# Kernel optimization log

Hardware: AMD Instinct MI355X
Metric: run time of the kernel (lower is better)

The kernel has to match this reference:

```python
import jax, jax.numpy as jnp
import numpy as np

EPS = 1e-8
LN_EPS = 1e-5

def _layernorm(x, g, b):
    mu = jnp.mean(x, axis=-1, keepdims=True)
    var = jnp.mean((x - mu) ** 2, axis=-1, keepdims=True)
    return (x - mu) / jnp.sqrt(var + LN_EPS) * g + b

def setup_inputs() -> dict:
    key = jax.random.key(0)
    ks = jax.random.split(key, 10)
    B, S = 8192, 4096
    input_dim, hidden_dim = 4, 256
    h4 = hidden_dim // 4  # 64
    price_series = jax.random.uniform(ks[0], (B, S, 1), dtype=jnp.float32) + 0.5
    # 4 parallel encoders stacked on leading axis: Linear(input_dim->h4) + LayerNorm(h4)
    enc_w = jax.random.normal(ks[1], (4, input_dim, h4), dtype=jnp.float32) * 0.5
    enc_b = jax.random.normal(ks[2], (4, h4), dtype=jnp.float32) * 0.02
    enc_g = jnp.ones((4, h4), dtype=jnp.float32)
    enc_beta = jnp.zeros((4, h4), dtype=jnp.float32)
    # regime head: Linear(hidden_dim->64) + ReLU + (Dropout eval=identity) + Linear(64->4)
    head_w1 = jax.random.normal(ks[3], (hidden_dim, 64), dtype=jnp.float32) * 0.0625
    head_b1 = jnp.zeros((64,), dtype=jnp.float32)
    head_w2 = jax.random.normal(ks[4], (64, 4), dtype=jnp.float32) * 0.125
    head_b2 = jnp.zeros((4,), dtype=jnp.float32)
    return {"price_series": price_series, "enc_w": enc_w, "enc_b": enc_b,
            "enc_g": enc_g, "enc_beta": enc_beta,
            "head_w1": head_w1, "head_b1": head_b1,
            "head_w2": head_w2, "head_b2": head_b2}

def reference(price_series, enc_w, enc_b, enc_g, enc_beta, head_w1, head_b1, head_w2, head_b2):
    prices = price_series[:, :, 0]  # [B, S]
    B, S = prices.shape
    # Rolling SMA(20) with clamped window start, via cumsum (single pass, no per-step loop)
    csum = jnp.concatenate([jnp.zeros((B, 1), prices.dtype), jnp.cumsum(prices, axis=1)], axis=1)  # [B, S+1]
    i = jnp.arange(S)
    start20 = jnp.maximum(0, i - 19)
    cnt20 = (i - start20 + 1).astype(prices.dtype)
    sma20 = (csum[:, i + 1] - csum[:, start20]) / cnt20  # [B, S]
    trend_signal = (prices - sma20) / (sma20 + EPS)
    f_trend = jnp.mean(trend_signal, axis=1, keepdims=True)  # [B,1]
    # momentum over last 10 steps
    p_last = prices[:, -1:]
    p_m10 = prices[:, -10:-9]
    f_mom = (p_last - p_m10) / (p_m10 + EPS)  # [B,1]
    # mean reversion
    p_mean = jnp.mean(prices, axis=1, keepdims=True)
    f_mr = (p_last - p_mean) / (p_mean + EPS)  # [B,1]
    # cycle: coefficient of variation (torch.std is unbiased, ddof=1)
    f_cyc = jnp.std(prices, axis=1, ddof=1, keepdims=True) / (p_mean + EPS)  # [B,1]
    combined = jnp.concatenate([f_trend, f_mom, f_mr, f_cyc], axis=1)  # [B, 4]
    # 4 parallel encoders: Linear -> ReLU -> LayerNorm
    pre = jnp.einsum('bi,eio->ebo', combined, enc_w) + enc_b[:, None, :]  # [4, B, 64]
    feats = _layernorm(jax.nn.relu(pre), enc_g[:, None, :], enc_beta[:, None, :])  # [4, B, 64]
    # concat order: trend, momentum, mean_rev, cycle along feature dim
    regime_features = jnp.transpose(feats, (1, 0, 2)).reshape(B, -1)  # [B, 256]
    h = jax.nn.relu(regime_features @ head_w1 + head_b1)
    regime_probs = jax.nn.softmax(h @ head_w2 + head_b2, axis=1)  # [B, 4]
    return (regime_features, regime_probs)
```

## Files before the change

kernel.cpp:

```cpp
#include <hip/hip_runtime.h>

#define EPS 1e-8f
#define LN_EPS 1e-5f
#define NROWS 8192
#define SLEN 4096
#define PROBS_OFF 2097152

typedef __attribute__((ext_vector_type(8))) short bf16x8;
typedef __attribute__((ext_vector_type(4))) float f32x4;

__device__ __forceinline__ short f2bf(float f) {
    unsigned u = __float_as_uint(f);
    unsigned r = (u + 0x7FFFu + ((u >> 16) & 1u)) >> 16;
    return (short)r;
}

#define SLP(i) ((i) + ((((i) >> 4)) << 2))

__global__ __launch_bounds__(256) void k_feat(const float* __restrict__ prices,
                                              float* __restrict__ ws) {
    __shared__ float sld[2596];
    __shared__ float red[12];

    const int t = threadIdx.x;
    const int b = blockIdx.x >> 1, h = blockIdx.x & 1;
    const int lane = t & 63, wv = t >> 6;
    const float4* rowp4 = (const float4*)(prices + (size_t)b * SLEN);

    {
        int f0 = t, f1 = t + 256;
        int g0 = 512 * h - 8 + f0, g1 = 512 * h - 8 + f1;
        float4 v0 = (g0 >= 0) ? rowp4[g0] : make_float4(0.f, 0.f, 0.f, 0.f);
        float4 v1 = rowp4[g1];
        *(float4*)&sld[SLP(4 * f0)] = v0;
        *(float4*)&sld[SLP(4 * f1)] = v1;
        if (t < 8) {
            int f2 = 512 + t;
            *(float4*)&sld[SLP(4 * f2)] = rowp4[512 * h - 8 + f2];
        }
    }
    __syncthreads();

    const int li0 = 32 + 8 * t;
    float4 s0 = *(const float4*)&sld[SLP(li0)];
    float4 s1 = *(const float4*)&sld[SLP(li0 + 4)];
    float4 q0 = *(const float4*)&sld[SLP(li0 - 20)];
    float4 q1 = *(const float4*)&sld[SLP(li0 - 16)];
    float4 q2 = *(const float4*)&sld[SLP(li0 - 12)];
    float4 q3 = *(const float4*)&sld[SLP(li0 - 8)];
    float4 q4 = *(const float4*)&sld[SLP(li0 - 4)];

    float xv[8] = { s0.x, s0.y, s0.z, s0.w, s1.x, s1.y, s1.z, s1.w };
    float ov[8] = { q0.x, q0.y, q0.z, q0.w, q1.x, q1.y, q1.z, q1.w };

    float W = q0.y + q0.z + q0.w
            + q1.x + q1.y + q1.z + q1.w
            + q2.x + q2.y + q2.z + q2.w
            + q3.x + q3.y + q3.z + q3.w
            + q4.x + q4.y + q4.z + q4.w;

    const float pf = (float)(2048 * h + 8 * t);
    float sum = 0.0f, sq = 0.0f, ts = 0.0f;
    #pragma unroll
    for (int j = 0; j < 8; ++j) {
        float x = xv[j];
        W += (j == 0) ? x : (x - ov[j]);
        sum += x;
        sq = fmaf(x, x, sq);
        float c = fminf(pf + (float)(j + 1), 20.0f);
        float num = fmaf(x, c, -W);
        float den = fmaf(EPS, c, W);
        ts += num * __builtin_amdgcn_rcpf(den);
    }

    if (h == 1 && t == 254) ws[(size_t)b * 8 + 6] = xv[6];
    if (h == 1 && t == 255) ws[(size_t)b * 8 + 7] = xv[7];

    #pragma unroll
    for (int off = 32; off > 0; off >>= 1) {
        sum += __shfl_xor(sum, off);
        sq  += __shfl_xor(sq,  off);
        ts  += __shfl_xor(ts,  off);
    }
    if (lane == 0) { red[wv * 3] = sum; red[wv * 3 + 1] = sq; red[wv * 3 + 2] = ts; }
    __syncthreads();

    if (t == 0) {
        float S = red[0] + red[3] + red[6] + red[9];
        float Q = red[1] + red[4] + red[7] + red[10];
        float T = red[2] + red[5] + red[8] + red[11];
        float* wp = ws + (size_t)b * 8 + 3 * h;
        wp[0] = S; wp[1] = Q; wp[2] = T;
    }
}

#define ROWS 32

__global__ __launch_bounds__(256) void k_head(
    const float* __restrict__ ws, float* __restrict__ out,
    const float* __restrict__ enc_w, const float* __restrict__ enc_b,
    const float* __restrict__ enc_g, const float* __restrict__ enc_bt,
    const float* __restrict__ w1, const float* __restrict__ b1,
    const float* __restrict__ w2, const float* __restrict__ b2)
{
    __shared__ float comb[ROWS][4];
    __shared__ short rfb[ROWS][264];
    __shared__ float hbuf[ROWS][68];

    const int t = threadIdx.x;
    const int r0 = blockIdx.x * ROWS;
    const int lane = t & 63, wave = t >> 6;
    const int l15 = lane & 15, q = lane >> 4;

    if (t < ROWS) {
        const float* wp = ws + (size_t)(r0 + t) * 8;
        float4 a = *(const float4*)wp;
        float4 bb = *(const float4*)(wp + 4);
        float S = a.x + a.w, Q = a.y + bb.x, T = a.z + bb.y;
        float p_m10 = bb.z, p_last = bb.w;
        float mean = S * (1.0f / 4096.0f);
        float var  = fmaxf((Q - 4096.0f * mean * mean) * (1.0f / 4095.0f), 0.0f);
        comb[t][0] = T * (1.0f / 4096.0f);
        comb[t][1] = (p_last - p_m10) / (p_m10 + EPS);
        comb[t][2] = (p_last - mean) / (mean + EPS);
        comb[t][3] = sqrtf(var) / (mean + EPS);
    }

    bf16x8 bfrag[8];
    #pragma unroll
    for (int kt = 0; kt < 8; ++kt) {
        #pragma unroll
        for (int j = 0; j < 8; ++j) {
            int k = kt * 32 + q * 8 + j;
            bfrag[kt][j] = f2bf(w1[k * 64 + wave * 16 + l15]);
        }
    }

    const float ew0 = enc_w[wave * 256 + lane];
    const float ew1v = enc_w[wave * 256 + 64 + lane];
    const float ew2v = enc_w[wave * 256 + 128 + lane];
    const float ew3v = enc_w[wave * 256 + 192 + lane];
    const float ebv = enc_b[t], egv = enc_g[t], btv = enc_bt[t];

    __syncthreads();

    for (int r = 0; r < ROWS; r += 2) {
        float4 cba = *(const float4*)comb[r];
        float4 cbb = *(const float4*)comb[r + 1];
        float va = fmaf(cba.x, ew0, fmaf(cba.y, ew1v, fmaf(cba.z, ew2v, fmaf(cba.w, ew3v, ebv))));
        float vb = fmaf(cbb.x, ew0, fmaf(cbb.y, ew1v, fmaf(cbb.z, ew2v, fmaf(cbb.w, ew3v, ebv))));
        va = fmaxf(va, 0.0f);
        vb = fmaxf(vb, 0.0f);
        float sma = va, smb = vb;
        #pragma unroll
        for (int off = 32; off > 0; off >>= 1) {
            sma += __shfl_xor(sma, off);
            smb += __shfl_xor(smb, off);
        }
        float mua = sma * (1.0f / 64.0f);
        float mub = smb * (1.0f / 64.0f);
        float da = va - mua, db = vb - mub;
        float vsa = da * da, vsb = db * db;
        #pragma unroll
        for (int off = 32; off > 0; off >>= 1) {
            vsa += __shfl_xor(vsa, off);
            vsb += __shfl_xor(vsb, off);
        }
        float ya = fmaf(da * rsqrtf(vsa * (1.0f / 64.0f) + LN_EPS), egv, btv);
        float yb = fmaf(db * rsqrtf(vsb * (1.0f / 64.0f) + LN_EPS), egv, btv);
        out[(size_t)(r0 + r) * 256 + t] = ya;
        out[(size_t)(r0 + r + 1) * 256 + t] = yb;
        rfb[r][t] = f2bf(ya);
        rfb[r + 1][t] = f2bf(yb);
    }
    __syncthreads();

    f32x4 acc0 = {0.f, 0.f, 0.f, 0.f}, acc1 = {0.f, 0.f, 0.f, 0.f};
    #pragma unroll
    for (int kt = 0; kt < 8; ++kt) {
        bf16x8 a0 = *(const bf16x8*)&rfb[l15][kt * 32 + q * 8];
        bf16x8 a1 = *(const bf16x8*)&rfb[16 + l15][kt * 32 + q * 8];
        acc0 = __builtin_amdgcn_mfma_f32_16x16x32_bf16(a0, bfrag[kt], acc0, 0, 0, 0);
        acc1 = __builtin_amdgcn_mfma_f32_16x16x32_bf16(a1, bfrag[kt], acc1, 0, 0, 0);
    }

    const int col = wave * 16 + l15;
    const float b1v = b1[col];
    #pragma unroll
    for (int rg = 0; rg < 4; ++rg) {
        hbuf[q * 4 + rg][col]      = fmaxf(acc0[rg] + b1v, 0.0f);
        hbuf[16 + q * 4 + rg][col] = fmaxf(acc1[rg] + b1v, 0.0f);
    }
    __syncthreads();

    if (t < 128) {
        int r = t >> 2, c = t & 3;
        float lg = b2[c];
        #pragma unroll
        for (int j = 0; j < 64; ++j) lg = fmaf(hbuf[r][j], w2[j * 4 + c], lg);
        float mx = fmaxf(lg, __shfl_xor(lg, 1, 4));
        mx = fmaxf(mx, __shfl_xor(mx, 2, 4));
        float ex = __expf(lg - mx);
        float s2 = ex + __shfl_xor(ex, 1, 4);
        s2 += __shfl_xor(s2, 2, 4);
        out[PROBS_OFF + (size_t)(r0 + r) * 4 + c] = ex / s2;
    }
}

extern "C" void kernel_launch(void* const* d_in, const int* in_sizes, int n_in,
                              void* d_out, int out_size, void* d_ws, size_t ws_size,
                              hipStream_t stream) {
    const float* prices  = (const float*)d_in[0];
    const float* enc_w   = (const float*)d_in[1];
    const float* enc_b   = (const float*)d_in[2];
    const float* enc_g   = (const float*)d_in[3];
    const float* enc_bt  = (const float*)d_in[4];
    const float* head_w1 = (const float*)d_in[5];
    const float* head_b1 = (const float*)d_in[6];
    const float* head_w2 = (const float*)d_in[7];
    const float* head_b2 = (const float*)d_in[8];
    float* out = (float*)d_out;
    float* ws  = (float*)d_ws;

    k_feat<<<NROWS * 2, 256, 0, stream>>>(prices, ws);
    k_head<<<NROWS / ROWS, 256, 0, stream>>>(ws, out, enc_w, enc_b, enc_g, enc_bt,
                                             head_w1, head_b1, head_w2, head_b2);
}
```

Before: 215.7 us.

## Process one row per feature block with direct global loads and fused finalize

The feature kernel now handles a full row per 512-thread block. Each thread reads its current and lookback float4s straight from global memory, relying on cache for the overlapping window loads instead of staging through LDS. The per-row feature finalization moves into this kernel, so the head kernel reads one float4 per row. The head kernel also shrinks to 16 rows per block with a single MFMA accumulator, doubling block count, and splits the w2 dot product into four independent chains. Redundant overlapping global loads may add cache traffic.

Result: slower. 307.1 us (+42.3%).

```diff
diff --git a/kernel.cpp b/kernel.cpp
--- a/kernel.cpp
+++ b/kernel.cpp
@@ -15,40 +15,24 @@
     return (short)r;
 }
 
-#define SLP(i) ((i) + ((((i) >> 4)) << 2))
-
-__global__ __launch_bounds__(256) void k_feat(const float* __restrict__ prices,
+__global__ __launch_bounds__(512) void k_feat(const float* __restrict__ prices,
                                               float* __restrict__ ws) {
-    __shared__ float sld[2596];
-    __shared__ float red[12];
+    __shared__ float red[8][3];
+    __shared__ float tailv[2];
 
     const int t = threadIdx.x;
-    const int b = blockIdx.x >> 1, h = blockIdx.x & 1;
+    const int b = blockIdx.x;
     const int lane = t & 63, wv = t >> 6;
-    const float4* rowp4 = (const float4*)(prices + (size_t)b * SLEN);
-
-    {
-        int f0 = t, f1 = t + 256;
-        int g0 = 512 * h - 8 + f0, g1 = 512 * h - 8 + f1;
-        float4 v0 = (g0 >= 0) ? rowp4[g0] : make_float4(0.f, 0.f, 0.f, 0.f);
-        float4 v1 = rowp4[g1];
-        *(float4*)&sld[SLP(4 * f0)] = v0;
-        *(float4*)&sld[SLP(4 * f1)] = v1;
-        if (t < 8) {
-            int f2 = 512 + t;
-            *(float4*)&sld[SLP(4 * f2)] = rowp4[512 * h - 8 + f2];
-        }
-    }
-    __syncthreads();
-
-    const int li0 = 32 + 8 * t;
-    float4 s0 = *(const float4*)&sld[SLP(li0)];
-    float4 s1 = *(const float4*)&sld[SLP(li0 + 4)];
-    float4 q0 = *(const float4*)&sld[SLP(li0 - 20)];
-    float4 q1 = *(const float4*)&sld[SLP(li0 - 16)];
-    float4 q2 = *(const float4*)&sld[SLP(li0 - 12)];
-    float4 q3 = *(const float4*)&sld[SLP(li0 - 8)];
-    float4 q4 = *(const float4*)&sld[SLP(li0 - 4)];
+    const float4* R4 = (const float4*)(prices + (size_t)b * SLEN);
+
+    const float4 z4 = make_float4(0.f, 0.f, 0.f, 0.f);
+    float4 s0 = R4[2 * t];
+    float4 s1 = R4[2 * t + 1];
+    float4 q0 = (2 * t - 5 >= 0) ? R4[2 * t - 5] : z4;
+    float4 q1 = (2 * t - 4 >= 0) ? R4[2 * t - 4] : z4;
+    float4 q2 = (2 * t - 3 >= 0) ? R4[2 * t - 3] : z4;
+    float4 q3 = (2 * t - 2 >= 0) ? R4[2 * t - 2] : z4;
+    float4 q4 = (2 * t - 1 >= 0) ? R4[2 * t - 1] : z4;
 
     float xv[8] = { s0.x, s0.y, s0.z, s0.w, s1.x, s1.y, s1.z, s1.w };
     float ov[8] = { q0.x, q0.y, q0.z, q0.w, q1.x, q1.y, q1.z, q1.w };
@@ -59,7 +43,7 @@
             + q3.x + q3.y + q3.z + q3.w
             + q4.x + q4.y + q4.z + q4.w;
 
-    const float pf = (float)(2048 * h + 8 * t);
+    const float pf = (float)(8 * t);
     float sum = 0.0f, sq = 0.0f, ts = 0.0f;
     #pragma unroll
     for (int j = 0; j < 8; ++j) {
@@ -73,8 +57,8 @@
         ts += num * __builtin_amdgcn_rcpf(den);
     }
 
-    if (h == 1 && t == 254) ws[(size_t)b * 8 + 6] = xv[6];
-    if (h == 1 && t == 255) ws[(size_t)b * 8 + 7] = xv[7];
+    if (t == 510) tailv[0] = xv[6];
+    if (t == 511) tailv[1] = xv[7];
 
     #pragma unroll
     for (int off = 32; off > 0; off >>= 1) {
@@ -82,19 +66,26 @@
         sq  += __shfl_xor(sq,  off);
         ts  += __shfl_xor(ts,  off);
     }
-    if (lane == 0) { red[wv * 3] = sum; red[wv * 3 + 1] = sq; red[wv * 3 + 2] = ts; }
+    if (lane == 0) { red[wv][0] = sum; red[wv][1] = sq; red[wv][2] = ts; }
     __syncthreads();
 
     if (t == 0) {
-        float S = red[0] + red[3] + red[6] + red[9];
-        float Q = red[1] + red[4] + red[7] + red[10];
-        float T = red[2] + red[5] + red[8] + red[11];
-        float* wp = ws + (size_t)b * 8 + 3 * h;
-        wp[0] = S; wp[1] = Q; wp[2] = T;
-    }
-}
-
-#define ROWS 32
+        float S = 0.f, Q = 0.f, T = 0.f;
+        #pragma unroll
+        for (int w = 0; w < 8; ++w) { S += red[w][0]; Q += red[w][1]; T += red[w][2]; }
+        float mean = S * (1.0f / 4096.0f);
+        float var  = fmaxf((Q - 4096.0f * mean * mean) * (1.0f / 4095.0f), 0.0f);
+        float p_m10 = tailv[0], p_last = tailv[1];
+        float4 f;
+        f.x = T * (1.0f / 4096.0f);
+        f.y = (p_last - p_m10) / (p_m10 + EPS);
+        f.z = (p_last - mean) / (mean + EPS);
+        f.w = sqrtf(var) / (mean + EPS);
+        ((float4*)ws)[b] = f;
+    }
+}
+
+#define ROWS 16
 
 __global__ __launch_bounds__(256) void k_head(
     const float* __restrict__ ws, float* __restrict__ out,
@@ -112,19 +103,7 @@
     const int lane = t & 63, wave = t >> 6;
     const int l15 = lane & 15, q = lane >> 4;
 
-    if (t < ROWS) {
-        const float* wp = ws + (size_t)(r0 + t) * 8;
-        float4 a = *(const float4*)wp;
-        float4 bb = *(const float4*)(wp + 4);
-        float S = a.x + a.w, Q = a.y + bb.x, T = a.z + bb.y;
-        float p_m10 = bb.z, p_last = bb.w;
-        float mean = S * (1.0f / 4096.0f);
-        float var  = fmaxf((Q - 4096.0f * mean * mean) * (1.0f / 4095.0f), 0.0f);
-        comb[t][0] = T * (1.0f / 4096.0f);
-        comb[t][1] = (p_last - p_m10) / (p_m10 + EPS);
-        comb[t][2] = (p_last - mean) / (mean + EPS);
-        comb[t][3] = sqrtf(var) / (mean + EPS);
-    }
+    if (t < ROWS) *(float4*)comb[t] = ((const float4*)ws)[r0 + t];
 
     bf16x8 bfrag[8];
     #pragma unroll
@@ -175,29 +154,31 @@
     }
     __syncthreads();
 
-    f32x4 acc0 = {0.f, 0.f, 0.f, 0.f}, acc1 = {0.f, 0.f, 0.f, 0.f};
+    f32x4 acc0 = {0.f, 0.f, 0.f, 0.f};
     #pragma unroll
     for (int kt = 0; kt < 8; ++kt) {
         bf16x8 a0 = *(const bf16x8*)&rfb[l15][kt * 32 + q * 8];
-        bf16x8 a1 = *(const bf16x8*)&rfb[16 + l15][kt * 32 + q * 8];
         acc0 = __builtin_amdgcn_mfma_f32_16x16x32_bf16(a0, bfrag[kt], acc0, 0, 0, 0);
-        acc1 = __builtin_amdgcn_mfma_f32_16x16x32_bf16(a1, bfrag[kt], acc1, 0, 0, 0);
     }
 
     const int col = wave * 16 + l15;
     const float b1v = b1[col];
     #pragma unroll
-    for (int rg = 0; rg < 4; ++rg) {
-        hbuf[q * 4 + rg][col]      = fmaxf(acc0[rg] + b1v, 0.0f);
-        hbuf[16 + q * 4 + rg][col] = fmaxf(acc1[rg] + b1v, 0.0f);
-    }
-    __syncthreads();
-
-    if (t < 128) {
+    for (int rg = 0; rg < 4; ++rg)
+        hbuf[q * 4 + rg][col] = fmaxf(acc0[rg] + b1v, 0.0f);
+    __syncthreads();
+
+    if (t < 4 * ROWS) {
         int r = t >> 2, c = t & 3;
-        float lg = b2[c];
-        #pragma unroll
-        for (int j = 0; j < 64; ++j) lg = fmaf(hbuf[r][j], w2[j * 4 + c], lg);
+        float a0 = 0.f, a1 = 0.f, a2 = 0.f, a3 = 0.f;
+        #pragma unroll
+        for (int j = 0; j < 16; ++j) {
+            a0 = fmaf(hbuf[r][j],      w2[j * 4 + c],        a0);
+            a1 = fmaf(hbuf[r][16 + j], w2[(16 + j) * 4 + c], a1);
+            a2 = fmaf(hbuf[r][32 + j], w2[(32 + j) * 4 + c], a2);
+            a3 = fmaf(hbuf[r][48 + j], w2[(48 + j) * 4 + c], a3);
+        }
+        float lg = b2[c] + ((a0 + a1) + (a2 + a3));
         float mx = fmaxf(lg, __shfl_xor(lg, 1, 4));
         mx = fmaxf(mx, __shfl_xor(mx, 2, 4));
         float ex = __expf(lg - mx);
@@ -222,7 +203,7 @@
     float* out = (float*)d_out;
     float* ws  = (float*)d_ws;
 
-    k_feat<<<NROWS * 2, 256, 0, stream>>>(prices, ws);
+    k_feat<<<NROWS, 512, 0, stream>>>(prices, ws);
     k_head<<<NROWS / ROWS, 256, 0, stream>>>(ws, out, enc_w, enc_b, enc_g, enc_bt,
                                              head_w1, head_b1, head_w2, head_b2);
 }
```
